# Kernel optimization log

Measured on AMD Instinct MI355X. Metric: run time of the kernel, lower is better.

## Reference

```python
import jax, jax.numpy as jnp
import numpy as np

K = 12  # nsample_k; graph per point has K nodes (self + K-1 abs-diff neighbors)


def setup_inputs() -> dict:
    key = jax.random.key(0)
    k1, k2, k3 = jax.random.split(key, 3)
    p = jax.random.normal(k1, (2, 8192, 3), dtype=jnp.float32)
    W = jax.random.normal(k2, (1, 3), dtype=jnp.float32) * 0.5  # GCNConv lin weight [out=1, in=3]
    b = jax.random.normal(k3, (1,), dtype=jnp.float32) * 0.1    # GCNConv bias
    return {"p": p, "W": W, "b": b}


def _knn_idx(pts, k):
    # k nearest neighbors over the whole flattened cloud, self included then dropped
    pts = jax.lax.stop_gradient(pts)  # indices are non-differentiable
    sq = jnp.sum(pts * pts, axis=-1)                      # [n]
    d2 = sq[:, None] + sq[None, :] - 2.0 * (pts @ pts.T)  # [n, n] squared distances
    _, idx = jax.lax.top_k(-d2, k)                        # ascending distance
    return idx[:, 1:]                                     # drop self -> [n, k-1]


def reference(p, W, b):
    # p: [B, N, 3] -> flatten to [n, 3]
    pts = p.reshape(-1, 3)
    nidx = _knn_idx(pts, K)            # [n, K-1]
    nbr = pts[nidx]                    # [n, K-1, 3]
    # node features of each star graph: node 0 = point, nodes 1..K-1 = |p - neighbor|
    p_ij = jnp.concatenate([pts[:, None, :], jnp.abs(pts[:, None, :] - nbr)], axis=1)  # [n, K, 3]
    # GCNConv(3,1) on identical star graphs (edges 0->j, plus self loops), closed form:
    #   deg0 = 1, deg_j = 2  =>  out0 = x0 W^T + b ; out_j = x0 W^T / sqrt(2) + x_j W^T / 2 + b
    xw = jnp.einsum('nkc,oc->nko', p_ij, W)  # [n, K, 1]
    inv_s2 = 1.0 / jnp.sqrt(jnp.float32(2.0))
    out0 = xw[:, :1] + b                                  # [n, 1, 1]
    outj = inv_s2 * xw[:, :1] + 0.5 * xw[:, 1:] + b       # [n, K-1, 1]
    emb = jnp.concatenate([out0, outj], axis=1)           # [n, K, 1]
    # POOL: squeeze -> [n, K]; AdaptiveAvgPool1d(1) -> [n, 1]; module returns avg only
    return jnp.mean(emb[..., 0], axis=1, keepdims=True)   # [n, 1]
```

## Files before the change

### kernel.cpp

```cpp
#include <hip/hip_runtime.h>
#include <math.h>


#define NBINS  2048
#define PARTS  16
#define CMIN_  (-6.0f)
#define INVBW_ ((float)NBINS / 12.0f)
#define BLOCK  256
#define WPB    4
#define SEED   768
#define KK     12
#define CD     4
#define BIG    3.0e38f

__device__ __forceinline__ int bin_of(float x) {
  int b = (int)((x - CMIN_) * INVBW_);
  b = b < 0 ? 0 : b;
  b = b > NBINS - 1 ? NBINS - 1 : b;
  return b;
}

__device__ __forceinline__ float wave_min(float v) {
#pragma unroll
  for (int o = 1; o < 64; o <<= 1) v = fminf(v, __shfl_xor(v, o));
  return v;
}

__device__ __forceinline__ void ins4(float (&qd)[CD], float (&qw)[CD],
                                     float d, float w) {
#pragma unroll
  for (int k = CD - 1; k >= 1; --k) {
    const bool up  = (qd[k - 1] > d);
    const bool mid = (qd[k] > d);
    const float nd = up ? qd[k - 1] : (mid ? d : qd[k]);
    const float nw = up ? qw[k - 1] : (mid ? w : qw[k]);
    qd[k] = nd; qw[k] = nw;
  }
  if (qd[0] > d) { qw[0] = w; qd[0] = d; }
}

__global__ __launch_bounds__(1024)
void sort_kernel(const float* __restrict__ p, int* __restrict__ c_all,
                 float4* __restrict__ s_all, int n) {
  __shared__ int h_all[NBINS];
  __shared__ int h_pre[NBINS];
  __shared__ int wsum[16];
  const int tid  = threadIdx.x;
  const int dim  = blockIdx.x / PARTS;
  const int part = blockIdx.x % PARTS;
  const int chunk   = (n + PARTS - 1) / PARTS;
  const int myStart = part * chunk;
  const int myEnd   = min(myStart + chunk, n);

  h_all[tid] = 0; h_all[tid + 1024] = 0;
  h_pre[tid] = 0; h_pre[tid + 1024] = 0;
  __syncthreads();

  for (int i = tid; i < n; i += 1024) {
    const int b = bin_of(p[3 * i + dim]);
    atomicAdd(&h_all[b], 1);
    if (i < myStart) atomicAdd(&h_pre[b], 1);
  }
  __syncthreads();

  const int a = h_all[2 * tid], b = h_all[2 * tid + 1];
  const int v = a + b;
  const int lane = tid & 63, wid = tid >> 6;
  int incl = v;
#pragma unroll
  for (int o = 1; o < 64; o <<= 1) {
    const int t = __shfl_up(incl, o);
    if (lane >= o) incl += t;
  }
  if (lane == 63) wsum[wid] = incl;
  __syncthreads();
  int woff = 0;
  for (int wI = 0; wI < wid; ++wI) woff += wsum[wI];
  const int excl = woff + incl - v;

  if (part == 0) {
    int* __restrict__ cursor = c_all + (size_t)dim * NBINS;
    cursor[2 * tid]     = excl + a;
    cursor[2 * tid + 1] = excl + a + b;
  }

  const int c0 = excl + h_pre[2 * tid];
  const int c1 = excl + a + h_pre[2 * tid + 1];
  __syncthreads();
  h_pre[2 * tid]     = c0;
  h_pre[2 * tid + 1] = c1;
  __syncthreads();

  float4* __restrict__ sorted = s_all + (size_t)dim * n;
  for (int i = myStart + tid; i < myEnd; i += 1024) {
    const float x = p[3 * i], y = p[3 * i + 1], z = p[3 * i + 2];
    const float c = (dim == 0) ? x : (dim == 1) ? y : z;
    const int pos = atomicAdd(&h_pre[bin_of(c)], 1);
    sorted[pos] = make_float4(x, y, z, __int_as_float(i));
  }
}

__global__ __launch_bounds__(BLOCK, 1)
void query_kernel(const float4* __restrict__ sx, const float4* __restrict__ sy,
                  const float4* __restrict__ sz, const int* __restrict__ cx,
                  const int* __restrict__ cy, const int* __restrict__ cz,
                  const float* __restrict__ W, const float* __restrict__ bias,
                  float* __restrict__ out, int n) {
  const int lane = threadIdx.x & 63;
  const int wv   = threadIdx.x >> 6;
  const int t    = wv * (n >> 2) + blockIdx.x;
  const float W0 = W[0], W1 = W[1], W2 = W[2];
  const float bb = bias[0];

  const float4 me = sx[t];
  const float xi = me.x, yi = me.y, zi = me.z;
  const int orig = __float_as_int(me.w);

  const float ax = fabsf(xi), ay = fabsf(yi), az = fabsf(zi);
  const float4* sv; const int* cur; float cq;
  if (ay >= ax && ay >= az)      { sv = sy; cur = cy; cq = yi; }
  else if (az >= ax && az >= ay) { sv = sz; cur = cz; cq = zi; }
  else                           { sv = sx; cur = cx; cq = xi; }

  const int bq = bin_of(cq);
  const int bs = (bq > 0) ? cur[bq - 1] : 0;
  const int be = cur[bq];
  int lo = ((bs + be) >> 1) - SEED / 2;
  lo = lo < 0 ? 0 : lo;
  lo = lo > n - SEED ? n - SEED : lo;
  const float4* base = sv + lo + lane;

  float4 cs[SEED / 64];
#pragma unroll
  for (int s = 0; s < SEED / 64; ++s) cs[s] = base[s * 64];
  __builtin_amdgcn_sched_barrier(0);
  float m0 = BIG, m1 = BIG, m2 = BIG, m3 = BIG;
#pragma unroll
  for (int s = 0; s < SEED / 64; s += 4) {
    {
      const float dx = xi - cs[s].x, dy = yi - cs[s].y, dz = zi - cs[s].z;
      m0 = fminf(m0, fmaf(dx, dx, fmaf(dy, dy, dz * dz)));
    }
    {
      const float dx = xi - cs[s + 1].x, dy = yi - cs[s + 1].y, dz = zi - cs[s + 1].z;
      m1 = fminf(m1, fmaf(dx, dx, fmaf(dy, dy, dz * dz)));
    }
    {
      const float dx = xi - cs[s + 2].x, dy = yi - cs[s + 2].y, dz = zi - cs[s + 2].z;
      m2 = fminf(m2, fmaf(dx, dx, fmaf(dy, dy, dz * dz)));
    }
    {
      const float dx = xi - cs[s + 3].x, dy = yi - cs[s + 3].y, dz = zi - cs[s + 3].z;
      m3 = fminf(m3, fmaf(dx, dx, fmaf(dy, dy, dz * dz)));
    }
  }
  const float m = fminf(fminf(m0, m1), fminf(m2, m3));

  float u;
  {
    float hiv = m;
#pragma unroll
    for (int o = 1; o < 64; o <<= 1) hiv = fmaxf(hiv, __shfl_xor(hiv, o));
    float lov = 0.f;
#pragma unroll
    for (int it = 0; it < 10; ++it) {
      const float mid = 0.5f * (lov + hiv);
      const int cnt = __popcll(__ballot(m <= mid));
      if (cnt >= KK) hiv = mid; else lov = mid;
    }
    u = hiv;
  }

  const float s = sqrtf(u);
  const int bl = bin_of(cq - s);
  const int bh = bin_of(cq + s);
  const int lo2 = (bl > 0) ? cur[bl - 1] : 0;
  const int hi2 = cur[bh];
  const int len   = hi2 - lo2;
  const int nch   = (len + 63) >> 6;
  const int steps = nch;

  float qd[CD], qw[CD];
  int ccnt = 0;
#pragma unroll
  for (int k = 0; k < CD; ++k) { qd[k] = BIG; qw[k] = 0.f; }

#define LD1(cix) (sv[lo2 + min((cix) * 64 + lane, len - 1)])
#define PROCC(cc, cix)                                                        \
  {                                                                           \
    const float dx = xi - (cc).x, dy = yi - (cc).y, dz = zi - (cc).z;         \
    float d2 = fmaf(dx, dx, fmaf(dy, dy, dz * dz));                           \
    d2 = ((cix) * 64 + lane < len) ? d2 : BIG;                                \
    if (d2 <= u) {                                                            \
      const float w = fmaf(W0, fabsf(dx), fmaf(W1, fabsf(dy), W2 * fabsf(dz)));\
      ++ccnt; ins4(qd, qw, d2, w);                                            \
    }                                                                         \
  }

  {
    float4 A0 = LD1(0), A1 = LD1(1), A2 = LD1(2), A3 = LD1(3);
    float4 B0, B1, B2, B3;
    int c = 0;
    for (;;) {
      B0 = LD1(c + 4); B1 = LD1(c + 5); B2 = LD1(c + 6); B3 = LD1(c + 7);
      PROCC(A0, c) PROCC(A1, c + 1) PROCC(A2, c + 2) PROCC(A3, c + 3)
      c += 4;
      if (c >= nch) break;
      A0 = LD1(c + 4); A1 = LD1(c + 5); A2 = LD1(c + 6); A3 = LD1(c + 7);
      PROCC(B0, c) PROCC(B1, c + 1) PROCC(B2, c + 2) PROCC(B3, c + 3)
      c += 4;
      if (c >= nch) break;
    }
  }
#undef LD1
#undef PROCC

  float acc = 0.f;
  const bool ovf = __ballot(ccnt > CD) != 0ULL;
  if (!ovf) {
#pragma unroll
    for (int r = 0; r < KK; ++r) {
      const float mm = wave_min(qd[0]);
      const unsigned long long bal = __ballot(qd[0] == mm);
      if (qd[0] == mm && lane == (int)(__ffsll(bal) - 1)) {
        acc += qw[0];
#pragma unroll
        for (int k = 0; k < CD - 1; ++k) { qd[k] = qd[k + 1]; qw[k] = qw[k + 1]; }
        qd[CD - 1] = BIG;
      }
    }
  } else {
    float dd[KK];
#pragma unroll
    for (int k = 0; k < KK; ++k) dd[k] = BIG;
    for (int s0 = 0; s0 < steps; ++s0) {
      const int pos = lo2 + s0 * 64 + lane;
      const float4 c = sv[(pos < hi2) ? pos : hi2 - 1];
      const float dx = xi - c.x, dy = yi - c.y, dz = zi - c.z;
      const float d2 = (pos < hi2) ? fmaf(dx, dx, fmaf(dy, dy, dz * dz)) : BIG;
#pragma unroll
      for (int k = KK - 1; k >= 1; --k)
        dd[k] = __builtin_amdgcn_fmed3f(d2, dd[k - 1], dd[k]);
      dd[0] = fminf(dd[0], d2);
    }
    float tau = 0.f;
#pragma unroll
    for (int r = 0; r < KK; ++r) {
      const float mm = wave_min(dd[0]);
      if (dd[0] == mm) {
#pragma unroll
        for (int k = 0; k < KK - 1; ++k) dd[k] = dd[k + 1];
        dd[KK - 1] = BIG;
      }
      tau = mm;
    }
    for (int s0 = 0; s0 < steps; ++s0) {
      const int pos = lo2 + s0 * 64 + lane;
      if (pos < hi2) {
        const float4 c = sv[pos];
        const float dx = xi - c.x, dy = yi - c.y, dz = zi - c.z;
        const float d2 = fmaf(dx, dx, fmaf(dy, dy, dz * dz));
        const float w  = fmaf(W0, fabsf(dx), fmaf(W1, fabsf(dy), W2 * fabsf(dz)));
        acc += (d2 <= tau) ? w : 0.f;
      }
    }
  }

#pragma unroll
  for (int o = 1; o < 64; o <<= 1) acc += __shfl_xor(acc, o);
  if (lane == 0) {
    const float xw0 = W0 * xi + W1 * yi + W2 * zi;
    out[orig] = bb + (xw0 * 8.778174593052022f + 0.5f * acc) * (1.0f / 12.0f);
  }
}

extern "C" void kernel_launch(void* const* d_in, const int* in_sizes, int n_in,
                              void* d_out, int out_size, void* d_ws, size_t ws_size,
                              hipStream_t stream) {
  const float* p  = (const float*)d_in[0];
  const float* W  = (const float*)d_in[1];
  const float* bb = (const float*)d_in[2];
  float* out = (float*)d_out;

  const int n = in_sizes[0] / 3;

  int*    c_all = (int*)d_ws;
  float4* s_all = (float4*)((char*)d_ws + 3 * NBINS * 4);
  int*    cx = c_all;
  int*    cy = cx + NBINS;
  int*    cz = cy + NBINS;
  float4* sx = s_all;
  float4* sy = sx + n;
  float4* sz = sy + n;

  sort_kernel<<<3 * PARTS, 1024, 0, stream>>>(p, c_all, s_all, n);
  query_kernel<<<n / WPB, BLOCK, 0, stream>>>(sx, sy, sz, cx, cy, cz, W, bb, out, n);
}
```

Measured before the change: 115.2 us.

## Reuse seed-window candidates in per-lane queues and skip reloading them in the candidate scan

The seed window's candidates now go straight into each lane's 4-deep top queue, and an eviction bound is tracked, instead of only computing a per-lane minimum. The later range scan then skips the seed window already processed, covering only the parts of [lo2,hi2) outside it. Overflow is detected after selection by comparing the smallest evicted distance with the final threshold, and only then falls back to the exact path. This removes duplicate loads and distance math, but every candidate now pays an unconditional insertion with no early filter against u, and the double-buffered prefetch loop is replaced by simple loops.

After: 109.6 us. 4.8% less time.

```diff
diff --git a/kernel.cpp b/kernel.cpp
--- a/kernel.cpp
+++ b/kernel.cpp
@@ -130,34 +130,33 @@
   lo = lo > n - SEED ? n - SEED : lo;
   const float4* base = sv + lo + lane;
 
-  float4 cs[SEED / 64];
-#pragma unroll
-  for (int s = 0; s < SEED / 64; ++s) cs[s] = base[s * 64];
-  __builtin_amdgcn_sched_barrier(0);
-  float m0 = BIG, m1 = BIG, m2 = BIG, m3 = BIG;
-#pragma unroll
-  for (int s = 0; s < SEED / 64; s += 4) {
-    {
-      const float dx = xi - cs[s].x, dy = yi - cs[s].y, dz = zi - cs[s].z;
-      m0 = fminf(m0, fmaf(dx, dx, fmaf(dy, dy, dz * dz)));
-    }
-    {
-      const float dx = xi - cs[s + 1].x, dy = yi - cs[s + 1].y, dz = zi - cs[s + 1].z;
-      m1 = fminf(m1, fmaf(dx, dx, fmaf(dy, dy, dz * dz)));
-    }
-    {
-      const float dx = xi - cs[s + 2].x, dy = yi - cs[s + 2].y, dz = zi - cs[s + 2].z;
-      m2 = fminf(m2, fmaf(dx, dx, fmaf(dy, dy, dz * dz)));
-    }
-    {
-      const float dx = xi - cs[s + 3].x, dy = yi - cs[s + 3].y, dz = zi - cs[s + 3].z;
-      m3 = fminf(m3, fmaf(dx, dx, fmaf(dy, dy, dz * dz)));
-    }
-  }
-  const float m = fminf(fminf(m0, m1), fminf(m2, m3));
+  float qd[CD], qw[CD];
+  float ev = BIG;
+#pragma unroll
+  for (int k = 0; k < CD; ++k) { qd[k] = BIG; qw[k] = 0.f; }
+
+#define PROCQ(cc, valid)                                                      \
+  {                                                                           \
+    const float dx = xi - (cc).x, dy = yi - (cc).y, dz = zi - (cc).z;         \
+    float d2 = fmaf(dx, dx, fmaf(dy, dy, dz * dz));                           \
+    d2 = (valid) ? d2 : BIG;                                                  \
+    const float w = fmaf(W0, fabsf(dx), fmaf(W1, fabsf(dy), W2 * fabsf(dz))); \
+    ev = fminf(ev, fmaxf(d2, qd[CD - 1]));                                    \
+    ins4(qd, qw, d2, w);                                                      \
+  }
+
+  {
+    float4 cs[SEED / 64];
+#pragma unroll
+    for (int s = 0; s < SEED / 64; ++s) cs[s] = base[s * 64];
+    __builtin_amdgcn_sched_barrier(0);
+#pragma unroll
+    for (int s = 0; s < SEED / 64; ++s) PROCQ(cs[s], true)
+  }
 
   float u;
   {
+    const float m = qd[0];
     float hiv = m;
 #pragma unroll
     for (int o = 1; o < 64; o <<= 1) hiv = fmaxf(hiv, __shfl_xor(hiv, o));
@@ -176,60 +175,47 @@
   const int bh = bin_of(cq + s);
   const int lo2 = (bl > 0) ? cur[bl - 1] : 0;
   const int hi2 = cur[bh];
-  const int len   = hi2 - lo2;
-  const int nch   = (len + 63) >> 6;
-  const int steps = nch;
-
-  float qd[CD], qw[CD];
-  int ccnt = 0;
-#pragma unroll
-  for (int k = 0; k < CD; ++k) { qd[k] = BIG; qw[k] = 0.f; }
-
-#define LD1(cix) (sv[lo2 + min((cix) * 64 + lane, len - 1)])
-#define PROCC(cc, cix)                                                        \
-  {                                                                           \
-    const float dx = xi - (cc).x, dy = yi - (cc).y, dz = zi - (cc).z;         \
-    float d2 = fmaf(dx, dx, fmaf(dy, dy, dz * dz));                           \
-    d2 = ((cix) * 64 + lane < len) ? d2 : BIG;                                \
-    if (d2 <= u) {                                                            \
-      const float w = fmaf(W0, fabsf(dx), fmaf(W1, fabsf(dy), W2 * fabsf(dz)));\
-      ++ccnt; ins4(qd, qw, d2, w);                                            \
-    }                                                                         \
-  }
-
-  {
-    float4 A0 = LD1(0), A1 = LD1(1), A2 = LD1(2), A3 = LD1(3);
-    float4 B0, B1, B2, B3;
-    int c = 0;
-    for (;;) {
-      B0 = LD1(c + 4); B1 = LD1(c + 5); B2 = LD1(c + 6); B3 = LD1(c + 7);
-      PROCC(A0, c) PROCC(A1, c + 1) PROCC(A2, c + 2) PROCC(A3, c + 3)
-      c += 4;
-      if (c >= nch) break;
-      A0 = LD1(c + 4); A1 = LD1(c + 5); A2 = LD1(c + 6); A3 = LD1(c + 7);
-      PROCC(B0, c) PROCC(B1, c + 1) PROCC(B2, c + 2) PROCC(B3, c + 3)
-      c += 4;
-      if (c >= nch) break;
-    }
-  }
-#undef LD1
-#undef PROCC
+  const int steps = (hi2 - lo2 + 63) >> 6;
+
+  {
+    const int a0 = lo2, b0 = min(hi2, lo);
+    const int len = b0 - a0;
+    const int nch = (len + 63) >> 6;
+    for (int c0 = 0; c0 < nch; ++c0) {
+      const int idx = c0 * 64 + lane;
+      const float4 c = sv[a0 + min(idx, len - 1)];
+      PROCQ(c, idx < len)
+    }
+  }
+  {
+    const int a0 = max(lo2, lo + SEED), b0 = hi2;
+    const int len = b0 - a0;
+    const int nch = (len + 63) >> 6;
+    for (int c0 = 0; c0 < nch; ++c0) {
+      const int idx = c0 * 64 + lane;
+      const float4 c = sv[a0 + min(idx, len - 1)];
+      PROCQ(c, idx < len)
+    }
+  }
+#undef PROCQ
 
   float acc = 0.f;
-  const bool ovf = __ballot(ccnt > CD) != 0ULL;
-  if (!ovf) {
-#pragma unroll
-    for (int r = 0; r < KK; ++r) {
-      const float mm = wave_min(qd[0]);
-      const unsigned long long bal = __ballot(qd[0] == mm);
-      if (qd[0] == mm && lane == (int)(__ffsll(bal) - 1)) {
-        acc += qw[0];
-#pragma unroll
-        for (int k = 0; k < CD - 1; ++k) { qd[k] = qd[k + 1]; qw[k] = qw[k + 1]; }
-        qd[CD - 1] = BIG;
-      }
-    }
-  } else {
+  float tau = 0.f;
+#pragma unroll
+  for (int r = 0; r < KK; ++r) {
+    const float mm = wave_min(qd[0]);
+    const unsigned long long bal = __ballot(qd[0] == mm);
+    if (qd[0] == mm && lane == (int)(__ffsll(bal) - 1)) {
+      acc += qw[0];
+#pragma unroll
+      for (int k = 0; k < CD - 1; ++k) { qd[k] = qd[k + 1]; qw[k] = qw[k + 1]; }
+      qd[CD - 1] = BIG;
+    }
+    tau = mm;
+  }
+
+  const bool ovf = __ballot(ev <= tau) != 0ULL;
+  if (ovf) {
     float dd[KK];
 #pragma unroll
     for (int k = 0; k < KK; ++k) dd[k] = BIG;
@@ -243,7 +229,7 @@
         dd[k] = __builtin_amdgcn_fmed3f(d2, dd[k - 1], dd[k]);
       dd[0] = fminf(dd[0], d2);
     }
-    float tau = 0.f;
+    float tau2 = 0.f;
 #pragma unroll
     for (int r = 0; r < KK; ++r) {
       const float mm = wave_min(dd[0]);
@@ -252,8 +238,9 @@
         for (int k = 0; k < KK - 1; ++k) dd[k] = dd[k + 1];
         dd[KK - 1] = BIG;
       }
-      tau = mm;
-    }
+      tau2 = mm;
+    }
+    acc = 0.f;
     for (int s0 = 0; s0 < steps; ++s0) {
       const int pos = lo2 + s0 * 64 + lane;
       if (pos < hi2) {
@@ -261,7 +248,7 @@
         const float dx = xi - c.x, dy = yi - c.y, dz = zi - c.z;
         const float d2 = fmaf(dx, dx, fmaf(dy, dy, dz * dz));
         const float w  = fmaf(W0, fabsf(dx), fmaf(W1, fabsf(dy), W2 * fabsf(dz)));
-        acc += (d2 <= tau) ? w : 0.f;
+        acc += (d2 <= tau2) ? w : 0.f;
       }
     }
   }
```
